# Optimization experiments

Measured on AMD Instinct MI355X. Metric: run time of the kernel, lower is better.

## Reference

```python
import jax, jax.numpy as jnp
import numpy as np

B, N, D = 8, 4096, 6          # clouds, points per cloud, coordinate dim
K = 64                        # max_num_neighbors in radius query
NS1, NS2 = 2048, 512          # fps ratios 0.5 and 0.25
R1, R2 = 0.2, 0.4             # ball-query radii
DIMS = {1: [6, 64, 64, 128], 2: [134, 128, 128, 256], 3: [262, 256, 512, 1024], 4: [1024, 512, 512]}


def setup_inputs():
    key = jax.random.key(0)
    k0, k1, k2 = jax.random.split(key, 3)
    inp = {}
    inp['synapse_cordi'] = jax.random.normal(k0, (B * N, D), jnp.float32)
    inp['batch_index'] = jnp.repeat(jnp.arange(B, dtype=jnp.int32), N)
    inp['weight'] = jax.random.uniform(k1, (B * N,), jnp.float32)
    k = k2
    for i, dims in DIMS.items():
        for j in range(len(dims) - 1):
            k, kw = jax.random.split(k)
            inp[f'w{i}_{j}'] = jax.random.normal(kw, (dims[j], dims[j + 1]), jnp.float32) * (1.0 / float(np.sqrt(dims[j])))
            inp[f'b{i}_{j}'] = jnp.zeros((dims[j + 1],), jnp.float32)
    return inp


def _mlp(x, params):
    # PyG MLP, plain_last=True; batch-norm at default (eval, running stats) is identity
    n = len(params)
    for i, (W, b) in enumerate(params):
        x = x @ W + b
        if i < n - 1:
            x = jax.nn.relu(x)
    return x


def _fps(pos, n_s):
    # farthest point sampling on one cloud [N, D] -> [n_s] indices (deterministic start at 0)
    d0 = jnp.sum((pos - pos[0]) ** 2, axis=-1)
    def step(mind, _):
        nxt = jnp.argmax(mind)
        mind = jnp.minimum(mind, jnp.sum((pos - pos[nxt]) ** 2, axis=-1))
        return mind, nxt
    _, idxs = jax.lax.scan(step, d0, None, length=n_s - 1)
    return jnp.concatenate([jnp.zeros((1,), idxs.dtype), idxs])


def _ball(pos, pos_q, r):
    # radius query: up to K nearest points within r for each query; [n_q,K] idx + validity mask
    d2 = jnp.sum((pos_q[:, None, :] - pos[None, :, :]) ** 2, axis=-1)  # [n_q, N]
    neg = jnp.where(d2 <= r * r, -d2, -jnp.inf)
    vals, nbr = jax.lax.top_k(neg, K)
    return nbr, vals > -jnp.inf


def _sa(x, pos, params, n_s, r):
    # Weight_Sample_Module: fps -> radius -> PointNetConv (gather, MLP, masked max-scatter)
    idx = jax.vmap(lambda p: _fps(p, n_s))(pos)                     # [B, n_s]
    pos_q = jnp.take_along_axis(pos, idx[..., None], axis=1)        # [B, n_s, D]
    nbr, valid = jax.vmap(lambda p, q: _ball(p, q, r))(pos, pos_q)  # [B, n_s, K]
    gather = lambda a: jax.vmap(lambda t, i: t[i])(a, nbr)          # [B, n_s, K, C]
    rel = gather(pos) - pos_q[:, :, None, :]
    feat = rel if x is None else jnp.concatenate([gather(x), rel], axis=-1)
    h = _mlp(feat, params)                                          # [B, n_s, K, C_out]
    h = jnp.where(valid[..., None], h, -jnp.inf)
    return jnp.max(h, axis=2), pos_q                                # max aggregation


def reference(synapse_cordi, batch_index, weight,
              w1_0, b1_0, w1_1, b1_1, w1_2, b1_2,
              w2_0, b2_0, w2_1, b2_1, w2_2, b2_2,
              w3_0, b3_0, w3_1, b3_1, w3_2, b3_2,
              w4_0, b4_0, w4_1, b4_1):
    pos = synapse_cordi.reshape(B, N, D)  # uniform clouds; batch_index = repeat(arange(B), N)
    p1 = [(w1_0, b1_0), (w1_1, b1_1), (w1_2, b1_2)]
    p2 = [(w2_0, b2_0), (w2_1, b2_1), (w2_2, b2_2)]
    p3 = [(w3_0, b3_0), (w3_1, b3_1), (w3_2, b3_2)]
    p4 = [(w4_0, b4_0), (w4_1, b4_1)]
    x1, pos1 = _sa(None, pos, p1, NS1, R1)   # [B, 2048, 128]
    x2, pos2 = _sa(x1, pos1, p2, NS2, R2)    # [B, 512, 256]
    h = _mlp(jnp.concatenate([x2, pos2], axis=-1), p3)  # [B, 512, 1024]
    g = jnp.max(h, axis=1)                   # global max pool -> [B, 1024]
    return _mlp(g, p4)                       # [B, 512]
```

## Files before the change

kernel.cpp:

```cpp
#include <hip/hip_runtime.h>
#include <math.h>

#define B_ 8
#define N_ 4096
#define D_ 6
#define K_ 64
#define NS1_ 2048
#define NS2_ 512

typedef float v2f __attribute__((ext_vector_type(2)));


__device__ __forceinline__ float dist2_rn(const float* __restrict__ a, const float* __restrict__ q) {
    float s = 0.f;
#pragma unroll
    for (int d = 0; d < 6; ++d) {
        float diff = __fsub_rn(a[d], q[d]);
        s = __fadd_rn(s, __fmul_rn(diff, diff));
    }
    return s;
}

__device__ __forceinline__ unsigned mapf(float x) {
    unsigned u = __float_as_uint(x);
    return (u & 0x80000000u) ? ~u : (u | 0x80000000u);
}
__device__ __forceinline__ float unmapf(unsigned u) {
    return __uint_as_float((u & 0x80000000u) ? (u & 0x7FFFFFFFu) : ~u);
}

template <int CTRL>
__device__ __forceinline__ double dppd(double k) {
    int lo = __double2loint(k), hi = __double2hiint(k);
    int nlo = __builtin_amdgcn_update_dpp(lo, lo, CTRL, 0xF, 0xF, false);
    int nhi = __builtin_amdgcn_update_dpp(hi, hi, CTRL, 0xF, 0xF, false);
    return __hiloint2double(nhi, nlo);
}


template <int NP, int NS, bool ZG>
__device__ __forceinline__ void fps_body(const float* __restrict__ p, float* __restrict__ posq,
                                         unsigned* __restrict__ g, float* __restrict__ spos,
                                         int* __restrict__ sidx, double* __restrict__ part, int t) {
#pragma clang fp contract(off)
    constexpr int NT = 256;
    constexpr int P = NP / NT;
    constexpr int HP = P / 2;
    int lane = t & 63, w = t >> 6;

    {
        const float4* src = (const float4*)p;
        float4* dst = (float4*)spos;
        for (int e = t; e < NP * 6 / 4; e += NT) dst[e] = src[e];
    }
    if (t == 0) sidx[0] = 0;
    __syncthreads();

    v2f px2[HP][6];
#pragma unroll
    for (int j = 0; j < HP; ++j)
#pragma unroll
        for (int d = 0; d < 6; ++d) {
            px2[j][d].x = spos[(t + NT * (2 * j)) * 6 + d];
            px2[j][d].y = spos[(t + NT * (2 * j + 1)) * 6 + d];
        }

    float cx[6];
#pragma unroll
    for (int d = 0; d < 6; ++d) cx[d] = spos[d];

    v2f mind2[HP];
    float runv = -1.f;
    int runj = 0;
#pragma unroll
    for (int j = 0; j < HP; ++j) {
        v2f d2 = {0.f, 0.f};
#pragma unroll
        for (int d = 0; d < 6; ++d) {
            v2f df = px2[j][d] - cx[d];
            d2 = d2 + df * df;
        }
        mind2[j] = d2;
        if (d2.x > runv) { runv = d2.x; runj = t + NT * (2 * j); }
        if (d2.y > runv) { runv = d2.y; runj = t + NT * (2 * j + 1); }
    }

    for (int s = 1; s < NS; ++s) {
        double key = __hiloint2double((int)__float_as_uint(runv), (int)(unsigned)(~runj));
        key = fmax(key, dppd<0x111>(key));
        key = fmax(key, dppd<0x112>(key));
        key = fmax(key, dppd<0x114>(key));
        key = fmax(key, dppd<0x118>(key));
        key = fmax(key, dppd<0x142>(key));
        key = fmax(key, dppd<0x143>(key));
        if (lane == 63) part[(s & 1) * 4 + w] = key;
        __syncthreads();
        double kk = part[(s & 1) * 4 + (lane & 3)];
        kk = fmax(kk, dppd<0x111>(kk));
        kk = fmax(kk, dppd<0x112>(kk));
        int nx = ~__builtin_amdgcn_readlane(__double2loint(kk), 3);
        if (t == 0) sidx[s] = nx;

        const float2* sv2 = (const float2*)spos;
        float2 ca = sv2[nx * 3], cb = sv2[nx * 3 + 1], cc = sv2[nx * 3 + 2];
        cx[0] = ca.x; cx[1] = ca.y; cx[2] = cb.x; cx[3] = cb.y; cx[4] = cc.x; cx[5] = cc.y;

        runv = -1.f;
        runj = 0;
#pragma unroll
        for (int j = 0; j < HP; ++j) {
            v2f d2 = {0.f, 0.f};
#pragma unroll
            for (int d = 0; d < 6; ++d) {
                v2f df = px2[j][d] - cx[d];
                d2 = d2 + df * df;
            }
            float mx = fminf(mind2[j].x, d2.x);
            float my = fminf(mind2[j].y, d2.y);
            mind2[j].x = mx;
            mind2[j].y = my;
            if (mx > runv) { runv = mx; runj = t + NT * (2 * j); }
            if (my > runv) { runv = my; runj = t + NT * (2 * j + 1); }
        }
    }
    __syncthreads();
    for (int s2 = t; s2 < NS; s2 += 256) {
        int nx = sidx[s2];
#pragma unroll
        for (int d = 0; d < 6; ++d) posq[(size_t)s2 * 6 + d] = spos[nx * 6 + d];
    }
    if (ZG) {
        for (int e = t; e < 1024; e += 256) g[e] = 0u;
    }
}


template <int S, int NPTS>
__device__ __forceinline__ void ball_body(const float* __restrict__ pos, const float* __restrict__ posq,
                                          int* __restrict__ nbr, int* __restrict__ cnt,
                                          int nq, float r2, int qid, int tid,
                                          float* __restrict__ sd, int* __restrict__ si) {
    int b = qid / nq;
    const float* p = pos + (size_t)b * NPTS * 6;
    float q[6];
#pragma unroll
    for (int d = 0; d < 6; ++d) q[d] = posq[(size_t)qid * 6 + d];

    int n = 0;
    float thr = INFINITY;
#pragma unroll 4
    for (int j = 0; j < NPTS; ++j) {
        float d2 = dist2_rn(p + (size_t)j * 6, q);
        if (d2 <= r2 && (n < K_ || d2 < thr)) {
            int i = (n < K_) ? n : (K_ - 1);
            if (n < K_) ++n;
            while (i > 0 && sd[(i - 1) * S + tid] > d2) {
                sd[i * S + tid] = sd[(i - 1) * S + tid];
                si[i * S + tid] = si[(i - 1) * S + tid];
                --i;
            }
            sd[i * S + tid] = d2;
            si[i * S + tid] = j;
            if (n == K_) thr = sd[(K_ - 1) * S + tid];
        }
    }
    cnt[qid] = n;
    for (int i = 0; i < n; ++i) nbr[(size_t)qid * K_ + i] = si[i * S + tid];
}


template <int NP, int NS>
__global__ __launch_bounds__(256, 1) void fps_kernel(const float* __restrict__ pos,
                                                     float* __restrict__ posq) {
    __shared__ float spos[NP * 6];
    __shared__ int sidx[NS];
    __shared__ double part[8];
    int b = blockIdx.x;
    fps_body<NP, NS, false>(pos + (size_t)b * NP * 6, posq + (size_t)b * NS * 6, nullptr,
                            spos, sidx, part, threadIdx.x);
}


__global__ __launch_bounds__(256, 1) void ball1_fps2_kernel(const float* __restrict__ pos,
                                                            const float* __restrict__ pos1,
                                                            int* __restrict__ nbr1, int* __restrict__ cnt1,
                                                            float* __restrict__ pos2,
                                                            unsigned* __restrict__ g, float r2) {
    __shared__ union SmemA {
        struct { float sd[K_ * 256]; int si[K_ * 256]; } ball;
        struct { float spos[NS1_ * 6]; int sidx[NS2_]; double part[8]; } fps;
    } sm;
    if (blockIdx.x < 64) {
        int qid = blockIdx.x * 256 + threadIdx.x;
        ball_body<256, N_>(pos, pos1, nbr1, cnt1, NS1_, r2, qid, threadIdx.x,
                           sm.ball.sd, sm.ball.si);
    } else {
        int b = blockIdx.x - 64;
        fps_body<NS1_, NS2_, true>(pos1 + (size_t)b * NS1_ * 6, pos2 + (size_t)b * NS2_ * 6,
                                   g + b * 1024, sm.fps.spos, sm.fps.sidx, sm.fps.part,
                                   threadIdx.x);
    }
}


__global__ __launch_bounds__(256) void sa1_ball2_kernel(const float* __restrict__ pos,
                                                        const float* __restrict__ pos1,
                                                        const int* __restrict__ nbr1,
                                                        const int* __restrict__ cnt1,
                                                        const float* __restrict__ W1, const float* __restrict__ B1,
                                                        const float* __restrict__ W2, const float* __restrict__ B2,
                                                        const float* __restrict__ W3, const float* __restrict__ B3,
                                                        float* __restrict__ x1,
                                                        const float* __restrict__ pos2,
                                                        int* __restrict__ nbr2, int* __restrict__ cnt2,
                                                        float r2_2) {
    __shared__ float sd[K_ * 64];
    __shared__ int si[K_ * 64];
    if (blockIdx.x >= 4096) {
        if (threadIdx.x >= 64) return;
        int qid = (blockIdx.x - 4096) * 64 + threadIdx.x;
        ball_body<64, NS1_>(pos1, pos2, nbr2, cnt2, NS2_, r2_2, qid, threadIdx.x, sd, si);
        return;
    }
    int lane = threadIdx.x & 63;
    int w = threadIdx.x >> 6;
    int qid = blockIdx.x * 4 + w;
    int b = qid / NS1_;
    const float* p = pos + (size_t)b * N_ * 6;
    float q[6];
#pragma unroll
    for (int d = 0; d < 6; ++d) q[d] = pos1[(size_t)qid * 6 + d];
    int c = cnt1[qid];
    float m0 = -INFINITY, m1 = -INFINITY;

    for (int n = 0; n < c; ++n) {
        int j = nbr1[(size_t)qid * K_ + n];
        float rel[6];
#pragma unroll
        for (int d = 0; d < 6; ++d) rel[d] = p[(size_t)j * 6 + d] - q[d];
        float a = B1[lane];
#pragma unroll
        for (int d = 0; d < 6; ++d) a = fmaf(W1[d * 64 + lane], rel[d], a);
        float h1 = fmaxf(a, 0.f);
        float a2 = B2[lane];
        for (int k = 0; k < 64; ++k) {
            float v = __shfl(h1, k, 64);
            a2 = fmaf(W2[k * 64 + lane], v, a2);
        }
        float h2 = fmaxf(a2, 0.f);
        float o0 = B3[lane], o1 = B3[64 + lane];
        for (int k = 0; k < 64; ++k) {
            float v = __shfl(h2, k, 64);
            o0 = fmaf(W3[k * 128 + lane], v, o0);
            o1 = fmaf(W3[k * 128 + 64 + lane], v, o1);
        }
        m0 = fmaxf(m0, o0);
        m1 = fmaxf(m1, o1);
    }
    x1[(size_t)qid * 128 + lane] = m0;
    x1[(size_t)qid * 128 + 64 + lane] = m1;
}


__global__ __launch_bounds__(256) void sa2_conv(const float* __restrict__ pos1, const float* __restrict__ posq,
                                                const int* __restrict__ nbr, const int* __restrict__ cnt,
                                                const float* __restrict__ x1,
                                                const float* __restrict__ W1, const float* __restrict__ B1,
                                                const float* __restrict__ W2, const float* __restrict__ B2,
                                                const float* __restrict__ W3, const float* __restrict__ B3,
                                                float* __restrict__ out) {
    int lane = threadIdx.x & 63;
    int w = threadIdx.x >> 6;
    int qid = blockIdx.x * 4 + w;
    int b = qid / NS2_;
    float q[6];
#pragma unroll
    for (int d = 0; d < 6; ++d) q[d] = posq[(size_t)qid * 6 + d];
    int c = cnt[qid];
    float m0 = -INFINITY, m1 = -INFINITY, m2 = -INFINITY, m3 = -INFINITY;

    for (int n = 0; n < c; ++n) {
        int j = nbr[(size_t)qid * K_ + n];
        size_t row = (size_t)b * NS1_ + j;
        const float* xs = x1 + row * 128;
        float rel[6];
#pragma unroll
        for (int d = 0; d < 6; ++d) rel[d] = pos1[row * 6 + d] - q[d];
        float a0 = B1[lane], a1 = B1[64 + lane];
        for (int k = 0; k < 128; ++k) {
            float v = xs[k];
            a0 = fmaf(W1[k * 128 + lane], v, a0);
            a1 = fmaf(W1[k * 128 + 64 + lane], v, a1);
        }
#pragma unroll
        for (int d = 0; d < 6; ++d) {
            float v = rel[d];
            a0 = fmaf(W1[(128 + d) * 128 + lane], v, a0);
            a1 = fmaf(W1[(128 + d) * 128 + 64 + lane], v, a1);
        }
        float h1a = fmaxf(a0, 0.f), h1b = fmaxf(a1, 0.f);
        float c0 = B2[lane], c1 = B2[64 + lane];
        for (int k = 0; k < 64; ++k) {
            float v = __shfl(h1a, k, 64);
            c0 = fmaf(W2[k * 128 + lane], v, c0);
            c1 = fmaf(W2[k * 128 + 64 + lane], v, c1);
        }
        for (int k = 0; k < 64; ++k) {
            float v = __shfl(h1b, k, 64);
            c0 = fmaf(W2[(64 + k) * 128 + lane], v, c0);
            c1 = fmaf(W2[(64 + k) * 128 + 64 + lane], v, c1);
        }
        float h2a = fmaxf(c0, 0.f), h2b = fmaxf(c1, 0.f);
        float e0 = B3[lane], e1 = B3[64 + lane], e2 = B3[128 + lane], e3 = B3[192 + lane];
        for (int k = 0; k < 64; ++k) {
            float v = __shfl(h2a, k, 64);
            e0 = fmaf(W3[k * 256 + lane], v, e0);
            e1 = fmaf(W3[k * 256 + 64 + lane], v, e1);
            e2 = fmaf(W3[k * 256 + 128 + lane], v, e2);
            e3 = fmaf(W3[k * 256 + 192 + lane], v, e3);
        }
        for (int k = 0; k < 64; ++k) {
            float v = __shfl(h2b, k, 64);
            e0 = fmaf(W3[(64 + k) * 256 + lane], v, e0);
            e1 = fmaf(W3[(64 + k) * 256 + 64 + lane], v, e1);
            e2 = fmaf(W3[(64 + k) * 256 + 128 + lane], v, e2);
            e3 = fmaf(W3[(64 + k) * 256 + 192 + lane], v, e3);
        }
        m0 = fmaxf(m0, e0);
        m1 = fmaxf(m1, e1);
        m2 = fmaxf(m2, e2);
        m3 = fmaxf(m3, e3);
    }
    out[(size_t)qid * 256 + lane] = m0;
    out[(size_t)qid * 256 + 64 + lane] = m1;
    out[(size_t)qid * 256 + 128 + lane] = m2;
    out[(size_t)qid * 256 + 192 + lane] = m3;
}


__global__ __launch_bounds__(256, 1) void mlp3_kernel(const float* __restrict__ x2, const float* __restrict__ pos2,
                                                      const float* __restrict__ W0, const float* __restrict__ B0,
                                                      const float* __restrict__ W1, const float* __restrict__ B1,
                                                      const float* __restrict__ W2, const float* __restrict__ B2,
                                                      unsigned* __restrict__ g) {
    int lane = threadIdx.x & 63;
    int w = threadIdx.x >> 6;
    int qid0 = blockIdx.x * 16 + w * 4;
    int b = qid0 >> 9;

    float xr[4][4];
#pragma unroll
    for (int q = 0; q < 4; ++q)
#pragma unroll
        for (int j = 0; j < 4; ++j) xr[q][j] = x2[(size_t)(qid0 + q) * 256 + j * 64 + lane];

    float a[4][4];
    {
        float4 bv = *(const float4*)&B0[lane * 4];
#pragma unroll
        for (int q = 0; q < 4; ++q) { a[q][0] = bv.x; a[q][1] = bv.y; a[q][2] = bv.z; a[q][3] = bv.w; }
    }
#pragma unroll
    for (int j = 0; j < 4; ++j) {
        for (int k2 = 0; k2 < 64; ++k2) {
            int k = j * 64 + k2;
            float4 wv = *(const float4*)&W0[(size_t)k * 256 + lane * 4];
#pragma unroll
            for (int q = 0; q < 4; ++q) {
                float v = __shfl(xr[q][j], k2, 64);
                a[q][0] = fmaf(wv.x, v, a[q][0]);
                a[q][1] = fmaf(wv.y, v, a[q][1]);
                a[q][2] = fmaf(wv.z, v, a[q][2]);
                a[q][3] = fmaf(wv.w, v, a[q][3]);
            }
        }
    }
#pragma unroll
    for (int d = 0; d < 6; ++d) {
        float4 wv = *(const float4*)&W0[(size_t)(256 + d) * 256 + lane * 4];
#pragma unroll
        for (int q = 0; q < 4; ++q) {
            float v = pos2[(size_t)(qid0 + q) * 6 + d];
            a[q][0] = fmaf(wv.x, v, a[q][0]);
            a[q][1] = fmaf(wv.y, v, a[q][1]);
            a[q][2] = fmaf(wv.z, v, a[q][2]);
            a[q][3] = fmaf(wv.w, v, a[q][3]);
        }
    }
    float h1[4][4];
#pragma unroll
    for (int q = 0; q < 4; ++q)
#pragma unroll
        for (int u = 0; u < 4; ++u) h1[q][u] = fmaxf(a[q][u], 0.f);

    float c[4][8];
    {
        float4 b0 = *(const float4*)&B1[lane * 8];
        float4 b1 = *(const float4*)&B1[lane * 8 + 4];
#pragma unroll
        for (int q = 0; q < 4; ++q) {
            c[q][0] = b0.x; c[q][1] = b0.y; c[q][2] = b0.z; c[q][3] = b0.w;
            c[q][4] = b1.x; c[q][5] = b1.y; c[q][6] = b1.z; c[q][7] = b1.w;
        }
    }
    for (int l = 0; l < 64; ++l) {
#pragma unroll
        for (int r = 0; r < 4; ++r) {
            int k = l * 4 + r;
            float4 w0 = *(const float4*)&W1[(size_t)k * 512 + lane * 8];
            float4 w1 = *(const float4*)&W1[(size_t)k * 512 + lane * 8 + 4];
#pragma unroll
            for (int q = 0; q < 4; ++q) {
                float v = __shfl(h1[q][r], l, 64);
                c[q][0] = fmaf(w0.x, v, c[q][0]);
                c[q][1] = fmaf(w0.y, v, c[q][1]);
                c[q][2] = fmaf(w0.z, v, c[q][2]);
                c[q][3] = fmaf(w0.w, v, c[q][3]);
                c[q][4] = fmaf(w1.x, v, c[q][4]);
                c[q][5] = fmaf(w1.y, v, c[q][5]);
                c[q][6] = fmaf(w1.z, v, c[q][6]);
                c[q][7] = fmaf(w1.w, v, c[q][7]);
            }
        }
    }
    float h2[4][8];
#pragma unroll
    for (int q = 0; q < 4; ++q)
#pragma unroll
        for (int u = 0; u < 8; ++u) h2[q][u] = fmaxf(c[q][u], 0.f);

    float e[4][16];
#pragma unroll
    for (int jj = 0; jj < 4; ++jj) {
        float4 bv = *(const float4*)&B2[lane * 16 + jj * 4];
#pragma unroll
        for (int q = 0; q < 4; ++q) {
            e[q][jj * 4 + 0] = bv.x; e[q][jj * 4 + 1] = bv.y;
            e[q][jj * 4 + 2] = bv.z; e[q][jj * 4 + 3] = bv.w;
        }
    }
    for (int l = 0; l < 64; ++l) {
#pragma unroll
        for (int r = 0; r < 8; ++r) {
            int k = l * 8 + r;
            const float* wp = &W2[(size_t)k * 1024 + lane * 16];
            float4 w0 = *(const float4*)&wp[0];
            float4 w1 = *(const float4*)&wp[4];
            float4 w2 = *(const float4*)&wp[8];
            float4 w3 = *(const float4*)&wp[12];
#pragma unroll
            for (int q = 0; q < 4; ++q) {
                float v = __shfl(h2[q][r], l, 64);
                e[q][0]  = fmaf(w0.x, v, e[q][0]);
                e[q][1]  = fmaf(w0.y, v, e[q][1]);
                e[q][2]  = fmaf(w0.z, v, e[q][2]);
                e[q][3]  = fmaf(w0.w, v, e[q][3]);
                e[q][4]  = fmaf(w1.x, v, e[q][4]);
                e[q][5]  = fmaf(w1.y, v, e[q][5]);
                e[q][6]  = fmaf(w1.z, v, e[q][6]);
                e[q][7]  = fmaf(w1.w, v, e[q][7]);
                e[q][8]  = fmaf(w2.x, v, e[q][8]);
                e[q][9]  = fmaf(w2.y, v, e[q][9]);
                e[q][10] = fmaf(w2.z, v, e[q][10]);
                e[q][11] = fmaf(w2.w, v, e[q][11]);
                e[q][12] = fmaf(w3.x, v, e[q][12]);
                e[q][13] = fmaf(w3.y, v, e[q][13]);
                e[q][14] = fmaf(w3.z, v, e[q][14]);
                e[q][15] = fmaf(w3.w, v, e[q][15]);
            }
        }
    }
#pragma unroll
    for (int u = 0; u < 16; ++u) {
        float m = fmaxf(fmaxf(e[0][u], e[1][u]), fmaxf(e[2][u], e[3][u]));
        atomicMax(&g[b * 1024 + lane * 16 + u], mapf(m));
    }
}


__global__ __launch_bounds__(512) void mlp4_kernel(const unsigned* __restrict__ g,
                                                   const float* __restrict__ W0, const float* __restrict__ B0,
                                                   const float* __restrict__ W1, const float* __restrict__ B1,
                                                   float* __restrict__ out) {
    int b = blockIdx.x;
    int c = threadIdx.x;
    __shared__ float h[512];
    float a = B0[c];
    for (int k = 0; k < 1024; ++k) {
        float v = unmapf(g[b * 1024 + k]);
        a = fmaf(v, W0[k * 512 + c], a);
    }
    h[c] = fmaxf(a, 0.f);
    __syncthreads();
    float o = B1[c];
    for (int k = 0; k < 512; ++k) o = fmaf(h[k], W1[k * 512 + c], o);
    out[(size_t)b * 512 + c] = o;
}


extern "C" void kernel_launch(void* const* d_in, const int* in_sizes, int n_in,
                              void* d_out, int out_size, void* d_ws, size_t ws_size,
                              hipStream_t stream) {
    const float* pos = (const float*)d_in[0];
    const float* w1_0 = (const float*)d_in[3];
    const float* b1_0 = (const float*)d_in[4];
    const float* w1_1 = (const float*)d_in[5];
    const float* b1_1 = (const float*)d_in[6];
    const float* w1_2 = (const float*)d_in[7];
    const float* b1_2 = (const float*)d_in[8];
    const float* w2_0 = (const float*)d_in[9];
    const float* b2_0 = (const float*)d_in[10];
    const float* w2_1 = (const float*)d_in[11];
    const float* b2_1 = (const float*)d_in[12];
    const float* w2_2 = (const float*)d_in[13];
    const float* b2_2 = (const float*)d_in[14];
    const float* w3_0 = (const float*)d_in[15];
    const float* b3_0 = (const float*)d_in[16];
    const float* w3_1 = (const float*)d_in[17];
    const float* b3_1 = (const float*)d_in[18];
    const float* w3_2 = (const float*)d_in[19];
    const float* b3_2 = (const float*)d_in[20];
    const float* w4_0 = (const float*)d_in[21];
    const float* b4_0 = (const float*)d_in[22];
    const float* w4_1 = (const float*)d_in[23];
    const float* b4_1 = (const float*)d_in[24];
    float* out = (float*)d_out;

    char* ws = (char*)d_ws;
    size_t off = 0;
    float* pos1 = (float*)(ws + off);  off += (size_t)B_ * NS1_ * 6 * 4;
    int* nbr1 = (int*)(ws + off);      off += (size_t)B_ * NS1_ * K_ * 4;
    int* cnt1 = (int*)(ws + off);      off += (size_t)B_ * NS1_ * 4;
    float* x1 = (float*)(ws + off);    off += (size_t)B_ * NS1_ * 128 * 4;
    float* pos2 = (float*)(ws + off);  off += (size_t)B_ * NS2_ * 6 * 4;
    int* nbr2 = (int*)(ws + off);      off += (size_t)B_ * NS2_ * K_ * 4;
    int* cnt2 = (int*)(ws + off);      off += (size_t)B_ * NS2_ * 4;
    float* x2 = (float*)(ws + off);    off += (size_t)B_ * NS2_ * 256 * 4;
    unsigned* g = (unsigned*)(ws + off); off += (size_t)B_ * 1024 * 4;

    const float r2_1 = (float)(0.2 * 0.2);
    const float r2_2 = (float)(0.4 * 0.4);

    fps_kernel<N_, NS1_><<<B_, 256, 0, stream>>>(pos, pos1);
    ball1_fps2_kernel<<<72, 256, 0, stream>>>(pos, pos1, nbr1, cnt1, pos2, g, r2_1);
    sa1_ball2_kernel<<<4096 + 64, 256, 0, stream>>>(pos, pos1, nbr1, cnt1,
                                                    w1_0, b1_0, w1_1, b1_1, w1_2, b1_2, x1,
                                                    pos2, nbr2, cnt2, r2_2);
    sa2_conv<<<(B_ * NS2_) / 4, 256, 0, stream>>>(pos1, pos2, nbr2, cnt2, x1,
                                                  w2_0, b2_0, w2_1, b2_1, w2_2, b2_2, x2);
    mlp3_kernel<<<(B_ * NS2_) / 16, 256, 0, stream>>>(x2, pos2, w3_0, b3_0, w3_1, b3_1, w3_2, b3_2, g);
    mlp4_kernel<<<B_, 512, 0, stream>>>(g, w4_0, b4_0, w4_1, b4_1, out);
}
```

Before: 2.877 ms.

## Pack two FPS clouds per 512-thread block and read centroids from global

Farthest point sampling now runs two clouds in one 512-thread block, using 4 blocks instead of 8 for stage 1 and 4 instead of 8 FPS blocks in the fused ball/FPS kernel. The LDS copy of the point cloud is removed, so points are loaded straight from global memory and each step's selected centroid is read from global (L1/L2) instead of LDS. Both clouds share one __syncthreads per step, which couples their progress, and the per-step centroid read moves from LDS to a cached global load on the serial critical path. In the fused kernel the ball-query blocks also become 512 threads, with the upper 256 threads exiting immediately.

```diff
diff --git a/kernel.cpp b/kernel.cpp
--- a/kernel.cpp
+++ b/kernel.cpp
@@ -39,35 +39,32 @@
 
 
 template <int NP, int NS, bool ZG>
-__device__ __forceinline__ void fps_body(const float* __restrict__ p, float* __restrict__ posq,
-                                         unsigned* __restrict__ g, float* __restrict__ spos,
-                                         int* __restrict__ sidx, double* __restrict__ part, int t) {
+__device__ __forceinline__ void fps_pair_body(const float* __restrict__ pos, float* __restrict__ posq,
+                                              unsigned* __restrict__ g, int c0,
+                                              int* __restrict__ sidx ,
+                                              double* __restrict__ part , int t) {
 #pragma clang fp contract(off)
-    constexpr int NT = 256;
-    constexpr int P = NP / NT;
+    constexpr int P = NP / 256;
     constexpr int HP = P / 2;
-    int lane = t & 63, w = t >> 6;
-
-    {
-        const float4* src = (const float4*)p;
-        float4* dst = (float4*)spos;
-        for (int e = t; e < NP * 6 / 4; e += NT) dst[e] = src[e];
-    }
-    if (t == 0) sidx[0] = 0;
-    __syncthreads();
+    int tloc = t & 255;
+    int cloud = t >> 8;
+    int lane = t & 63, ww = (t >> 6) & 3;
+    const float* p = pos + (size_t)(c0 + cloud) * NP * 6;
+    float* pq = posq + (size_t)(c0 + cloud) * NS * 6;
 
     v2f px2[HP][6];
 #pragma unroll
-    for (int j = 0; j < HP; ++j)
-#pragma unroll
-        for (int d = 0; d < 6; ++d) {
-            px2[j][d].x = spos[(t + NT * (2 * j)) * 6 + d];
-            px2[j][d].y = spos[(t + NT * (2 * j + 1)) * 6 + d];
-        }
+    for (int j = 0; j < HP; ++j) {
+        const float* pa = p + (size_t)(tloc + 256 * (2 * j)) * 6;
+        const float* pb = p + (size_t)(tloc + 256 * (2 * j + 1)) * 6;
+#pragma unroll
+        for (int d = 0; d < 6; ++d) { px2[j][d].x = pa[d]; px2[j][d].y = pb[d]; }
+    }
+    if (tloc == 0) sidx[cloud * NS] = 0;
 
     float cx[6];
 #pragma unroll
-    for (int d = 0; d < 6; ++d) cx[d] = spos[d];
+    for (int d = 0; d < 6; ++d) cx[d] = p[d];
 
     v2f mind2[HP];
     float runv = -1.f;
@@ -81,8 +78,8 @@
             d2 = d2 + df * df;
         }
         mind2[j] = d2;
-        if (d2.x > runv) { runv = d2.x; runj = t + NT * (2 * j); }
-        if (d2.y > runv) { runv = d2.y; runj = t + NT * (2 * j + 1); }
+        if (d2.x > runv) { runv = d2.x; runj = tloc + 256 * (2 * j); }
+        if (d2.y > runv) { runv = d2.y; runj = tloc + 256 * (2 * j + 1); }
     }
 
     for (int s = 1; s < NS; ++s) {
@@ -93,17 +90,17 @@
         key = fmax(key, dppd<0x118>(key));
         key = fmax(key, dppd<0x142>(key));
         key = fmax(key, dppd<0x143>(key));
-        if (lane == 63) part[(s & 1) * 4 + w] = key;
+        if (lane == 63) part[(cloud * 2 + (s & 1)) * 4 + ww] = key;
         __syncthreads();
-        double kk = part[(s & 1) * 4 + (lane & 3)];
+        double kk = part[(cloud * 2 + (s & 1)) * 4 + (lane & 3)];
         kk = fmax(kk, dppd<0x111>(kk));
         kk = fmax(kk, dppd<0x112>(kk));
         int nx = ~__builtin_amdgcn_readlane(__double2loint(kk), 3);
-        if (t == 0) sidx[s] = nx;
-
-        const float2* sv2 = (const float2*)spos;
-        float2 ca = sv2[nx * 3], cb = sv2[nx * 3 + 1], cc = sv2[nx * 3 + 2];
-        cx[0] = ca.x; cx[1] = ca.y; cx[2] = cb.x; cx[3] = cb.y; cx[4] = cc.x; cx[5] = cc.y;
+        if (tloc == 0) sidx[cloud * NS + s] = nx;
+
+        const float* pc = p + (size_t)nx * 6;
+#pragma unroll
+        for (int d = 0; d < 6; ++d) cx[d] = pc[d];
 
         runv = -1.f;
         runj = 0;
@@ -119,18 +116,19 @@
             float my = fminf(mind2[j].y, d2.y);
             mind2[j].x = mx;
             mind2[j].y = my;
-            if (mx > runv) { runv = mx; runj = t + NT * (2 * j); }
-            if (my > runv) { runv = my; runj = t + NT * (2 * j + 1); }
+            if (mx > runv) { runv = mx; runj = tloc + 256 * (2 * j); }
+            if (my > runv) { runv = my; runj = tloc + 256 * (2 * j + 1); }
         }
     }
     __syncthreads();
-    for (int s2 = t; s2 < NS; s2 += 256) {
-        int nx = sidx[s2];
-#pragma unroll
-        for (int d = 0; d < 6; ++d) posq[(size_t)s2 * 6 + d] = spos[nx * 6 + d];
+    for (int s2 = tloc; s2 < NS; s2 += 256) {
+        int nx = sidx[cloud * NS + s2];
+        const float* pc = p + (size_t)nx * 6;
+#pragma unroll
+        for (int d = 0; d < 6; ++d) pq[(size_t)s2 * 6 + d] = pc[d];
     }
     if (ZG) {
-        for (int e = t; e < 1024; e += 256) g[e] = 0u;
+        for (int e = tloc; e < 1024; e += 256) g[(c0 + cloud) * 1024 + e] = 0u;
     }
 }
 
@@ -170,35 +168,31 @@
 
 
 template <int NP, int NS>
-__global__ __launch_bounds__(256, 1) void fps_kernel(const float* __restrict__ pos,
+__global__ __launch_bounds__(512, 1) void fps_kernel(const float* __restrict__ pos,
                                                      float* __restrict__ posq) {
-    __shared__ float spos[NP * 6];
-    __shared__ int sidx[NS];
-    __shared__ double part[8];
-    int b = blockIdx.x;
-    fps_body<NP, NS, false>(pos + (size_t)b * NP * 6, posq + (size_t)b * NS * 6, nullptr,
-                            spos, sidx, part, threadIdx.x);
-}
-
-
-__global__ __launch_bounds__(256, 1) void ball1_fps2_kernel(const float* __restrict__ pos,
+    __shared__ int sidx[2 * NS];
+    __shared__ double part[16];
+    fps_pair_body<NP, NS, false>(pos, posq, nullptr, blockIdx.x * 2, sidx, part, threadIdx.x);
+}
+
+
+__global__ __launch_bounds__(512, 1) void ball1_fps2_kernel(const float* __restrict__ pos,
                                                             const float* __restrict__ pos1,
                                                             int* __restrict__ nbr1, int* __restrict__ cnt1,
                                                             float* __restrict__ pos2,
                                                             unsigned* __restrict__ g, float r2) {
     __shared__ union SmemA {
         struct { float sd[K_ * 256]; int si[K_ * 256]; } ball;
-        struct { float spos[NS1_ * 6]; int sidx[NS2_]; double part[8]; } fps;
+        struct { int sidx[2 * NS2_]; double part[16]; } fps;
     } sm;
     if (blockIdx.x < 64) {
+        if (threadIdx.x >= 256) return;
         int qid = blockIdx.x * 256 + threadIdx.x;
         ball_body<256, N_>(pos, pos1, nbr1, cnt1, NS1_, r2, qid, threadIdx.x,
                            sm.ball.sd, sm.ball.si);
     } else {
-        int b = blockIdx.x - 64;
-        fps_body<NS1_, NS2_, true>(pos1 + (size_t)b * NS1_ * 6, pos2 + (size_t)b * NS2_ * 6,
-                                   g + b * 1024, sm.fps.spos, sm.fps.sidx, sm.fps.part,
-                                   threadIdx.x);
+        fps_pair_body<NS1_, NS2_, true>(pos1, pos2, g, (blockIdx.x - 64) * 2,
+                                        sm.fps.sidx, sm.fps.part, threadIdx.x);
     }
 }
 
@@ -541,8 +535,8 @@
     const float r2_1 = (float)(0.2 * 0.2);
     const float r2_2 = (float)(0.4 * 0.4);
 
-    fps_kernel<N_, NS1_><<<B_, 256, 0, stream>>>(pos, pos1);
-    ball1_fps2_kernel<<<72, 256, 0, stream>>>(pos, pos1, nbr1, cnt1, pos2, g, r2_1);
+    fps_kernel<N_, NS1_><<<B_ / 2, 512, 0, stream>>>(pos, pos1);
+    ball1_fps2_kernel<<<68, 512, 0, stream>>>(pos, pos1, nbr1, cnt1, pos2, g, r2_1);
     sa1_ball2_kernel<<<4096 + 64, 256, 0, stream>>>(pos, pos1, nbr1, cnt1,
                                                     w1_0, b1_0, w1_1, b1_1, w1_2, b1_2, x1,
                                                     pos2, nbr2, cnt2, r2_2);
```

After: 4.004 ms. +39.2%, slower.

## Replace first FPS kernel with 512-thread-per-cloud spin-synchronised version

Applied to the files above, without the earlier changes.

The first farthest-point-sampling stage now runs two clouds per 1024-thread block, giving each cloud 512 threads so each thread holds fewer points in registers. The per-step __syncthreads barrier is replaced by a per-cloud LDS atomic counter that waves spin on, with a double-buffered partial-max array. Point coordinates are no longer staged in LDS; the selected centroid is read from global memory. This aims to cut the per-iteration latency of the serial 2047-step loop, at the cost of spin-wait overhead and uncached global reads.

```diff
diff --git a/kernel.cpp b/kernel.cpp
--- a/kernel.cpp
+++ b/kernel.cpp
@@ -38,8 +38,115 @@
 }
 
 
+template <int NP, int NS>
+__global__ __launch_bounds__(1024, 4) void fps_spin_kernel(const float* __restrict__ pos,
+                                                           float* __restrict__ posq) {
+#pragma clang fp contract(off)
+    constexpr int CT = 512;
+    constexpr int P = NP / CT;
+    constexpr int HP = P / 2;
+    int t = threadIdx.x;
+    int cloud = t >> 9;
+    int tloc = t & 511;
+    int lane = t & 63, w8 = (tloc >> 6);
+    int b = blockIdx.x * 2 + cloud;
+    const float* p = pos + (size_t)b * NP * 6;
+    float* pq = posq + (size_t)b * NS * 6;
+
+    __shared__ double part[2][2][8];
+    __shared__ int scnt[2];
+    __shared__ int sidx[2][NS];
+
+    if (t < 2) scnt[t] = 0;
+    if (tloc == 0) sidx[cloud][0] = 0;
+    __syncthreads();
+
+    v2f px2[HP][6];
+#pragma unroll
+    for (int j = 0; j < HP; ++j) {
+        const float* pa = p + (size_t)(tloc + CT * (2 * j)) * 6;
+        const float* pb = p + (size_t)(tloc + CT * (2 * j + 1)) * 6;
+#pragma unroll
+        for (int d = 0; d < 6; ++d) { px2[j][d].x = pa[d]; px2[j][d].y = pb[d]; }
+    }
+
+    float cx[6];
+#pragma unroll
+    for (int d = 0; d < 6; ++d) cx[d] = p[d];
+
+    v2f mind2[HP];
+    float runv = -1.f;
+    int runj = 0;
+#pragma unroll
+    for (int j = 0; j < HP; ++j) {
+        v2f d2 = {0.f, 0.f};
+#pragma unroll
+        for (int d = 0; d < 6; ++d) {
+            v2f df = px2[j][d] - cx[d];
+            d2 = d2 + df * df;
+        }
+        mind2[j] = d2;
+        if (d2.x > runv) { runv = d2.x; runj = tloc + CT * (2 * j); }
+        if (d2.y > runv) { runv = d2.y; runj = tloc + CT * (2 * j + 1); }
+    }
+
+    for (int s = 1; s < NS; ++s) {
+        double key = __hiloint2double((int)__float_as_uint(runv), (int)(unsigned)(~runj));
+        key = fmax(key, dppd<0x111>(key));
+        key = fmax(key, dppd<0x112>(key));
+        key = fmax(key, dppd<0x114>(key));
+        key = fmax(key, dppd<0x118>(key));
+        key = fmax(key, dppd<0x142>(key));
+        key = fmax(key, dppd<0x143>(key));
+        if (lane == 63) {
+            part[cloud][s & 1][w8] = key;
+            __hip_atomic_fetch_add(&scnt[cloud], 1, __ATOMIC_RELEASE, __HIP_MEMORY_SCOPE_WORKGROUP);
+        }
+        int target = 8 * s;
+        while (__hip_atomic_load(&scnt[cloud], __ATOMIC_ACQUIRE, __HIP_MEMORY_SCOPE_WORKGROUP) < target) {
+            __builtin_amdgcn_s_sleep(1);
+        }
+        double kk = part[cloud][s & 1][lane & 7];
+        kk = fmax(kk, dppd<0x111>(kk));
+        kk = fmax(kk, dppd<0x112>(kk));
+        kk = fmax(kk, dppd<0x114>(kk));
+        int nx = ~__builtin_amdgcn_readlane(__double2loint(kk), 7);
+        if (tloc == 0) sidx[cloud][s] = nx;
+
+        const float* pc = p + (size_t)nx * 6;
+#pragma unroll
+        for (int d = 0; d < 6; ++d) cx[d] = pc[d];
+
+        runv = -1.f;
+        runj = 0;
+#pragma unroll
+        for (int j = 0; j < HP; ++j) {
+            v2f d2 = {0.f, 0.f};
+#pragma unroll
+            for (int d = 0; d < 6; ++d) {
+                v2f df = px2[j][d] - cx[d];
+                d2 = d2 + df * df;
+            }
+            float mx = fminf(mind2[j].x, d2.x);
+            float my = fminf(mind2[j].y, d2.y);
+            mind2[j].x = mx;
+            mind2[j].y = my;
+            if (mx > runv) { runv = mx; runj = tloc + CT * (2 * j); }
+            if (my > runv) { runv = my; runj = tloc + CT * (2 * j + 1); }
+        }
+    }
+    __syncthreads();
+    for (int s2 = tloc; s2 < NS; s2 += CT) {
+        int nx = sidx[cloud][s2];
+        const float* pc = p + (size_t)nx * 6;
+#pragma unroll
+        for (int d = 0; d < 6; ++d) pq[(size_t)s2 * 6 + d] = pc[d];
+    }
+}
+
+
 template <int NP, int NS, bool ZG>
-__device__ __forceinline__ void fps_body(const float* __restrict__ p, float* __restrict__ posq,
+__device__ __forceinline__ void fps_body(const float* __restrict__ p, float* __restrict__ pq,
                                          unsigned* __restrict__ g, float* __restrict__ spos,
                                          int* __restrict__ sidx, double* __restrict__ part, int t) {
 #pragma clang fp contract(off)
@@ -124,13 +231,13 @@
         }
     }
     __syncthreads();
-    for (int s2 = t; s2 < NS; s2 += 256) {
+    for (int s2 = t; s2 < NS; s2 += NT) {
         int nx = sidx[s2];
 #pragma unroll
-        for (int d = 0; d < 6; ++d) posq[(size_t)s2 * 6 + d] = spos[nx * 6 + d];
+        for (int d = 0; d < 6; ++d) pq[(size_t)s2 * 6 + d] = spos[nx * 6 + d];
     }
     if (ZG) {
-        for (int e = t; e < 1024; e += 256) g[e] = 0u;
+        for (int e = t; e < 1024; e += NT) g[e] = 0u;
     }
 }
 
@@ -166,18 +273,6 @@
     }
     cnt[qid] = n;
     for (int i = 0; i < n; ++i) nbr[(size_t)qid * K_ + i] = si[i * S + tid];
-}
-
-
-template <int NP, int NS>
-__global__ __launch_bounds__(256, 1) void fps_kernel(const float* __restrict__ pos,
-                                                     float* __restrict__ posq) {
-    __shared__ float spos[NP * 6];
-    __shared__ int sidx[NS];
-    __shared__ double part[8];
-    int b = blockIdx.x;
-    fps_body<NP, NS, false>(pos + (size_t)b * NP * 6, posq + (size_t)b * NS * 6, nullptr,
-                            spos, sidx, part, threadIdx.x);
 }
 
 
@@ -541,7 +636,7 @@
     const float r2_1 = (float)(0.2 * 0.2);
     const float r2_2 = (float)(0.4 * 0.4);
 
-    fps_kernel<N_, NS1_><<<B_, 256, 0, stream>>>(pos, pos1);
+    fps_spin_kernel<N_, NS1_><<<B_ / 2, 1024, 0, stream>>>(pos, pos1);
     ball1_fps2_kernel<<<72, 256, 0, stream>>>(pos, pos1, nbr1, cnt1, pos2, g, r2_1);
     sa1_ball2_kernel<<<4096 + 64, 256, 0, stream>>>(pos, pos1, nbr1, cnt1,
                                                     w1_0, b1_0, w1_1, b1_1, w1_2, b1_2, x1,
```

Result: slower. 4.159 ms (+44.6%).
